# Kernel optimization log

Hardware: AMD Instinct MI355X
Metric: run time of the kernel (lower is better)

The kernel has to match this reference:

```python
import jax, jax.numpy as jnp
import numpy as np

N_NODES = 100000
N_EDGES = 1600000
DIM = 64
L = 5
NUM_GRAPHS = 256
BN_EPS = 1e-5


def setup_inputs() -> dict:
    key = jax.random.key(0)
    ks = jax.random.split(key, 8)
    x = jax.random.normal(ks[0], (N_NODES, DIM), dtype=jnp.float32)
    edge_index = jax.random.randint(ks[1], (2, N_EDGES), 0, N_NODES, dtype=jnp.int32).astype(jnp.int64)
    batch = jnp.sort(jax.random.randint(ks[2], (N_NODES,), 0, NUM_GRAPHS, dtype=jnp.int32)).astype(jnp.int64)
    W1 = jax.random.normal(ks[3], (L, DIM, DIM), dtype=jnp.float32) * (1.0 / np.sqrt(DIM))
    b1 = jnp.zeros((L, DIM), dtype=jnp.float32)
    W2 = jax.random.normal(ks[4], (L, DIM, DIM), dtype=jnp.float32) * (1.0 / np.sqrt(DIM))
    b2 = jnp.zeros((L, DIM), dtype=jnp.float32)
    gamma = jnp.ones((L, DIM), dtype=jnp.float32)
    beta = jnp.zeros((L, DIM), dtype=jnp.float32)
    return {"x": x, "edge_index": edge_index, "batch": batch, "W1": W1, "b1": b1, "W2": W2, "b2": b2, "gamma": gamma, "beta": beta}


def reference(x, edge_index, batch, W1, b1, W2, b2, gamma, beta):
    src, dst = edge_index[0], edge_index[1]
    n = x.shape[0]
    h = x
    xs = []
    for i in range(L):
        # GINConv (eps=0): h_i' = MLP(h_i + sum_{j->i} h_j), scatter-add over edges
        agg = jax.ops.segment_sum(h[src], dst, num_segments=n)
        z = h + agg
        z = jnp.maximum(z @ W1[i] + b1[i], 0.0) @ W2[i] + b2[i]
        z = jnp.maximum(z, 0.0)  # outer ReLU
        # BatchNorm1d, training-mode batch stats (biased var)
        mu = jnp.mean(z, axis=0)
        var = jnp.mean((z - mu) ** 2, axis=0)
        z = (z - mu) * jax.lax.rsqrt(var + BN_EPS) * gamma[i] + beta[i]
        xs.append(z)
        h = z
    counts = jax.ops.segment_sum(jnp.ones((n,), dtype=x.dtype), batch, num_segments=NUM_GRAPHS)
    counts = jnp.maximum(counts, 1.0)[:, None]
    xpool = [jax.ops.segment_sum(z, batch, num_segments=NUM_GRAPHS) / counts for z in xs]
    return jnp.concatenate(xpool, axis=1), jnp.concatenate(xs, axis=1)
```

## Files before the change

### kernel.cpp

```cpp
#include <hip/hip_runtime.h>

#define N_NODES 100000
#define N_EDGES 1600000
#define DIM 64
#define NLAYERS 5
#define NUM_GRAPHS 256
#define BN_EPS 1e-5f
#define STATS_BLOCKS 256
#define CSR_CAP 32
#define OV_CAP 65536
#define NSHARD 4
#define SHARD_W (N_NODES / NSHARD)
#define NBLK ((N_NODES + 255) / 256)

__global__ __launch_bounds__(256) void build_csr_shard_kernel(
        const int* __restrict__ ei, int* __restrict__ cursor,
        int* __restrict__ csr, int* __restrict__ ovcnt, int* __restrict__ ovpairs,
        int lo, int hi) {
    int e = blockIdx.x * 256 + threadIdx.x;
    if (e >= N_EDGES) return;
    int t = ei[N_EDGES + e];
    if (t < lo || t >= hi) return;
    int s = ei[e];
    int c = atomicAdd(&cursor[t], 1);
    if (c < CSR_CAP) {
        csr[t * CSR_CAP + c] = s;
    } else {
        int o = atomicAdd(ovcnt, 1);
        if (o < OV_CAP) { ovpairs[2 * o] = t; ovpairs[2 * o + 1] = s; }
    }
}

__global__ void pad_csr_kernel(const int* __restrict__ cursor, int* __restrict__ csr) {
    int n = blockIdx.x * 256 + threadIdx.x;
    if (n >= N_NODES) return;
    int cnt = min(cursor[n], CSR_CAP);
    int cnt8 = (cnt + 7) & ~7;
    for (int k = cnt; k < cnt8; ++k) csr[n * CSR_CAP + k] = 0;
}

__global__ __launch_bounds__(256) void aggregate_kernel(
        const int* __restrict__ csr, const int* __restrict__ deg,
        const int* __restrict__ ovcnt, const int* __restrict__ ovpairs,
        const float* __restrict__ h, int hstride, float* __restrict__ agg) {
    long tid = (long)blockIdx.x * 256 + threadIdx.x;
    int n = (int)(tid >> 6);
    int d = (int)(tid & 63);
    if (n >= N_NODES) return;
    int dval = deg[n];
    int cnt = min(dval, CSR_CAP);
    int cnt8 = (cnt + 7) & ~7;
    const int4* row = (const int4*)(csr + n * CSR_CAP);
    float own = h[(long)n * hstride + d];
    float a0 = 0.f, a1 = 0.f, a2 = 0.f, a3 = 0.f;
    float a4 = 0.f, a5 = 0.f, a6 = 0.f, a7 = 0.f;
    for (int k = 0; k < cnt8; k += 8) {
        int4 ra = row[k >> 2];
        int4 rb = row[(k >> 2) + 1];
        float v0 = h[(long)ra.x * hstride + d];
        float v1 = h[(long)ra.y * hstride + d];
        float v2 = h[(long)ra.z * hstride + d];
        float v3 = h[(long)ra.w * hstride + d];
        float v4 = h[(long)rb.x * hstride + d];
        float v5 = h[(long)rb.y * hstride + d];
        float v6 = h[(long)rb.z * hstride + d];
        float v7 = h[(long)rb.w * hstride + d];
        if (k + 0 < cnt) a0 += v0;
        if (k + 1 < cnt) a1 += v1;
        if (k + 2 < cnt) a2 += v2;
        if (k + 3 < cnt) a3 += v3;
        if (k + 4 < cnt) a4 += v4;
        if (k + 5 < cnt) a5 += v5;
        if (k + 6 < cnt) a6 += v6;
        if (k + 7 < cnt) a7 += v7;
    }
    if (dval > CSR_CAP) {
        int m = min(*ovcnt, OV_CAP);
        for (int i = 0; i < m; ++i) {
            if (ovpairs[2 * i] == n) a0 += h[(long)ovpairs[2 * i + 1] * hstride + d];
        }
    }
    agg[(long)n * DIM + d] = own + ((a0 + a1) + (a2 + a3)) + ((a4 + a5) + (a6 + a7));
}

__global__ __launch_bounds__(256) void mlp_gemm_kernel(
        const float* __restrict__ in, const float* __restrict__ W,
        const float* __restrict__ b, float* __restrict__ out) {
    __shared__ __align__(16) float sW[DIM * DIM];
    __shared__ float sb[DIM];
    for (int k = threadIdx.x; k < DIM * DIM / 4; k += 256)
        ((float4*)sW)[k] = ((const float4*)W)[k];
    if (threadIdx.x < DIM) sb[threadIdx.x] = b[threadIdx.x];
    __syncthreads();

    int p = threadIdx.x & 127;
    int j0 = (threadIdx.x >> 7) * 32;
    int base = blockIdx.x * 256;
    int n0 = base + p;
    int n1 = base + 128 + p;
    bool v1 = n1 < N_NODES;
    const float* inr0 = in + (long)n0 * DIM;
    const float* inr1 = in + (long)(v1 ? n1 : n0) * DIM;

    float acc0[32], acc1[32];
#pragma unroll
    for (int j = 0; j < 32; ++j) { acc0[j] = sb[j0 + j]; acc1[j] = acc0[j]; }

    for (int d4 = 0; d4 < DIM / 4; ++d4) {
        float4 za = ((const float4*)inr0)[d4];
        float4 zb = ((const float4*)inr1)[d4];
        const float* w0 = sW + (d4 * 4 + 0) * DIM + j0;
        const float* w1 = sW + (d4 * 4 + 1) * DIM + j0;
        const float* w2 = sW + (d4 * 4 + 2) * DIM + j0;
        const float* w3 = sW + (d4 * 4 + 3) * DIM + j0;
#pragma unroll
        for (int j = 0; j < 32; j += 4) {
            float4 a0 = *(const float4*)(w0 + j);
            float4 a1 = *(const float4*)(w1 + j);
            float4 a2 = *(const float4*)(w2 + j);
            float4 a3 = *(const float4*)(w3 + j);
            acc0[j + 0] += za.x * a0.x + za.y * a1.x + za.z * a2.x + za.w * a3.x;
            acc0[j + 1] += za.x * a0.y + za.y * a1.y + za.z * a2.y + za.w * a3.y;
            acc0[j + 2] += za.x * a0.z + za.y * a1.z + za.z * a2.z + za.w * a3.z;
            acc0[j + 3] += za.x * a0.w + za.y * a1.w + za.z * a2.w + za.w * a3.w;
            acc1[j + 0] += zb.x * a0.x + zb.y * a1.x + zb.z * a2.x + zb.w * a3.x;
            acc1[j + 1] += zb.x * a0.y + zb.y * a1.y + zb.z * a2.y + zb.w * a3.y;
            acc1[j + 2] += zb.x * a0.z + zb.y * a1.z + zb.z * a2.z + zb.w * a3.z;
            acc1[j + 3] += zb.x * a0.w + zb.y * a1.w + zb.z * a2.w + zb.w * a3.w;
        }
    }

    float* o0 = out + (long)n0 * DIM + j0;
#pragma unroll
    for (int j = 0; j < 32; j += 4) {
        float4 v = { fmaxf(acc0[j], 0.f), fmaxf(acc0[j + 1], 0.f),
                     fmaxf(acc0[j + 2], 0.f), fmaxf(acc0[j + 3], 0.f) };
        *(float4*)(o0 + j) = v;
    }
    if (v1) {
        float* o1 = out + (long)n1 * DIM + j0;
#pragma unroll
        for (int j = 0; j < 32; j += 4) {
            float4 v = { fmaxf(acc1[j], 0.f), fmaxf(acc1[j + 1], 0.f),
                         fmaxf(acc1[j + 2], 0.f), fmaxf(acc1[j + 3], 0.f) };
            *(float4*)(o1 + j) = v;
        }
    }
}

__global__ void stats_partial_kernel(const float* __restrict__ z, float* __restrict__ partials) {
    __shared__ float red[2 * 256];
    int d = threadIdx.x & 63;
    int slot = threadIdx.x >> 6;
    const int S = STATS_BLOCKS * 4;
    float s1 = 0.f, s2 = 0.f;
    int n = blockIdx.x * 4 + slot;
    for (; n + 3 * S < N_NODES; n += 4 * S) {
        float v0 = z[(long)(n + 0 * S) * DIM + d];
        float v1 = z[(long)(n + 1 * S) * DIM + d];
        float v2 = z[(long)(n + 2 * S) * DIM + d];
        float v3 = z[(long)(n + 3 * S) * DIM + d];
        s1 += v0 + v1 + v2 + v3;
        s2 += v0 * v0 + v1 * v1 + v2 * v2 + v3 * v3;
    }
    for (; n < N_NODES; n += S) {
        float v = z[(long)n * DIM + d];
        s1 += v;
        s2 += v * v;
    }
    red[threadIdx.x] = s1;
    red[256 + threadIdx.x] = s2;
    __syncthreads();
    if (threadIdx.x < 64) {
        float a = red[d] + red[64 + d] + red[128 + d] + red[192 + d];
        float c = red[256 + d] + red[320 + d] + red[384 + d] + red[448 + d];
        partials[blockIdx.x * 128 + d] = a;
        partials[blockIdx.x * 128 + 64 + d] = c;
    }
}

__global__ void stats_finalize_kernel(const float* __restrict__ partials,
                                      const float* __restrict__ gamma,
                                      const float* __restrict__ beta,
                                      float* __restrict__ ss) {
    __shared__ float r1[256], r2[256];
    int d = threadIdx.x & 63, q = threadIdx.x >> 6;
    float s1 = 0.f, s2 = 0.f;
    for (int b2_ = q; b2_ < STATS_BLOCKS; b2_ += 4) {
        s1 += partials[b2_ * 128 + d];
        s2 += partials[b2_ * 128 + 64 + d];
    }
    r1[threadIdx.x] = s1;
    r2[threadIdx.x] = s2;
    __syncthreads();
    if (threadIdx.x < 64) {
        s1 = r1[d] + r1[64 + d] + r1[128 + d] + r1[192 + d];
        s2 = r2[d] + r2[64 + d] + r2[128 + d] + r2[192 + d];
        float mu = s1 * (1.f / N_NODES);
        float var = s2 * (1.f / N_NODES) - mu * mu;
        float rs = 1.f / sqrtf(fmaxf(var, 0.f) + BN_EPS);
        float sc = gamma[d] * rs;
        ss[d] = sc;
        ss[64 + d] = beta[d] - mu * sc;
    }
}

__global__ void bn_apply_kernel(const float* __restrict__ z, const float* __restrict__ ss,
                                float* __restrict__ outxs) {
    long t = (long)blockIdx.x * 256 + threadIdx.x;
    if (t >= (long)N_NODES * (DIM / 4)) return;
    int r = (int)(t & 15);
    long n = t >> 4;
    float4 v = ((const float4*)(z + n * DIM))[r];
    float4 sc = ((const float4*)ss)[r];
    float4 sh = ((const float4*)(ss + DIM))[r];
    float4 o = { v.x * sc.x + sh.x, v.y * sc.y + sh.y,
                 v.z * sc.z + sh.z, v.w * sc.w + sh.w };
    ((float4*)(outxs + n * (DIM * NLAYERS)))[r] = o;
}

__global__ void graph_starts_kernel(const int* __restrict__ batch, int* __restrict__ starts) {
    int g = threadIdx.x;
    if (g > NUM_GRAPHS) return;
    int lo = 0, hi = N_NODES;
    while (lo < hi) {
        int mid = (lo + hi) >> 1;
        if (batch[mid] < g) lo = mid + 1; else hi = mid;
    }
    starts[g] = lo;
}

__global__ void pool_kernel(const float* __restrict__ xs, const int* __restrict__ starts,
                            float* __restrict__ outpool) {
    int g = blockIdx.x;
    int d = threadIdx.x;
    int s = starts[g], e = starts[g + 1];
    const int LD = DIM * NLAYERS;
    float a0 = 0.f, a1 = 0.f, a2 = 0.f, a3 = 0.f;
    float a4 = 0.f, a5 = 0.f, a6 = 0.f, a7 = 0.f;
    int n = s;
    for (; n + 8 <= e; n += 8) {
        a0 += xs[(long)(n + 0) * LD + d];
        a1 += xs[(long)(n + 1) * LD + d];
        a2 += xs[(long)(n + 2) * LD + d];
        a3 += xs[(long)(n + 3) * LD + d];
        a4 += xs[(long)(n + 4) * LD + d];
        a5 += xs[(long)(n + 5) * LD + d];
        a6 += xs[(long)(n + 6) * LD + d];
        a7 += xs[(long)(n + 7) * LD + d];
    }
    for (; n < e; ++n) a0 += xs[(long)n * LD + d];
    float acc = ((a0 + a1) + (a2 + a3)) + ((a4 + a5) + (a6 + a7));
    outpool[(long)g * LD + d] = acc / fmaxf((float)(e - s), 1.f);
}

static inline size_t rup(size_t x) { return (x + 255) & ~(size_t)255; }

extern "C" void kernel_launch(void* const* d_in, const int* in_sizes, int n_in,
                              void* d_out, int out_size, void* d_ws, size_t ws_size,
                              hipStream_t stream) {
    const float* x     = (const float*)d_in[0];
    const int*   ei    = (const int*)d_in[1];
    const int*   batch = (const int*)d_in[2];
    const float* W1    = (const float*)d_in[3];
    const float* b1    = (const float*)d_in[4];
    const float* W2    = (const float*)d_in[5];
    const float* b2    = (const float*)d_in[6];
    const float* gamma = (const float*)d_in[7];
    const float* beta  = (const float*)d_in[8];

    float* out      = (float*)d_out;
    float* out_pool = out;
    float* out_xs   = out + (size_t)NUM_GRAPHS * DIM * NLAYERS;

    char* w = (char*)d_ws;
    int*   csr      = (int*)w;    w += rup((size_t)N_NODES * CSR_CAP * 4);
    int*   cursor   = (int*)w;    w += rup((size_t)N_NODES * 4);
    int*   ovcnt    = (int*)w;    w += 256;
    int*   ovpairs  = (int*)w;    w += rup((size_t)OV_CAP * 8);
    float* agg      = (float*)w;  w += rup((size_t)N_NODES * DIM * 4);
    float* bufB     = (float*)w;  w += rup((size_t)N_NODES * DIM * 4);
    float* partials = (float*)w;  w += rup((size_t)STATS_BLOCKS * 128 * 4);
    float* ss       = (float*)w;  w += 512;
    int*   starts   = (int*)w;    w += rup((size_t)(NUM_GRAPHS + 1) * 4);

    hipMemsetAsync(cursor, 0, (size_t)N_NODES * 4, stream);
    hipMemsetAsync(ovcnt, 0, 4, stream);
    for (int sh = 0; sh < NSHARD; ++sh) {
        build_csr_shard_kernel<<<(N_EDGES + 255) / 256, 256, 0, stream>>>(
            ei, cursor, csr, ovcnt, ovpairs, sh * SHARD_W, (sh + 1) * SHARD_W);
    }
    pad_csr_kernel<<<NBLK, 256, 0, stream>>>(cursor, csr);
    graph_starts_kernel<<<1, 320, 0, stream>>>(batch, starts);

    const float* h = x;
    int hs = DIM;
    for (int l = 0; l < NLAYERS; ++l) {
        aggregate_kernel<<<((long)N_NODES * DIM + 255) / 256, 256, 0, stream>>>(
            csr, cursor, ovcnt, ovpairs, h, hs, agg);
        mlp_gemm_kernel<<<NBLK, 256, 0, stream>>>(
            agg, W1 + (size_t)l * DIM * DIM, b1 + (size_t)l * DIM, bufB);
        mlp_gemm_kernel<<<NBLK, 256, 0, stream>>>(
            bufB, W2 + (size_t)l * DIM * DIM, b2 + (size_t)l * DIM, agg);
        stats_partial_kernel<<<STATS_BLOCKS, 256, 0, stream>>>(agg, partials);
        stats_finalize_kernel<<<1, 256, 0, stream>>>(partials, gamma + (size_t)l * DIM,
                                                     beta + (size_t)l * DIM, ss);
        bn_apply_kernel<<<((long)N_NODES * (DIM / 4) + 255) / 256, 256, 0, stream>>>(
            agg, ss, out_xs + (size_t)l * DIM);
        h = out_xs + (size_t)l * DIM;
        hs = DIM * NLAYERS;
    }

    pool_kernel<<<NUM_GRAPHS, 320, 0, stream>>>(out_xs, starts, out_pool);
}
```

Measured before the change: 960.0 us.

## Aggregate from feature-sliced node layout with one wave per node-slice

Node features are stored in a slice-major layout (8 slices of 8 floats per node), written by a new transpose kernel for the input and by the BN apply kernel for later layers. Aggregation runs one wavefront per node and slice: eight lanes per neighbour group each gather 8 contiguous floats, and the partial sums are combined with cross-lane shuffles. The aim is to keep each slice's gather working set small enough to stay in cache and to load the CSR row once instead of per feature. The padding kernel is dropped because indices are now masked, and the pool kernel is split across layers into more blocks. The cost is an extra layout buffer, extra writes in BN apply, and one block per four nodes per slice.

```diff
diff --git a/kernel.cpp b/kernel.cpp
--- a/kernel.cpp
+++ b/kernel.cpp
@@ -12,6 +12,7 @@
 #define NSHARD 4
 #define SHARD_W (N_NODES / NSHARD)
 #define NBLK ((N_NODES + 255) / 256)
+#define NSLICE 8
 
 __global__ __launch_bounds__(256) void build_csr_shard_kernel(
         const int* __restrict__ ei, int* __restrict__ cursor,
@@ -31,56 +32,71 @@
     }
 }
 
-__global__ void pad_csr_kernel(const int* __restrict__ cursor, int* __restrict__ csr) {
-    int n = blockIdx.x * 256 + threadIdx.x;
-    if (n >= N_NODES) return;
-    int cnt = min(cursor[n], CSR_CAP);
-    int cnt8 = (cnt + 7) & ~7;
-    for (int k = cnt; k < cnt8; ++k) csr[n * CSR_CAP + k] = 0;
-}
-
-__global__ __launch_bounds__(256) void aggregate_kernel(
+__global__ void transpose_x_kernel(const float* __restrict__ x, float* __restrict__ hb) {
+    long t = (long)blockIdx.x * 256 + threadIdx.x;
+    if (t >= (long)N_NODES * DIM) return;
+    int n = (int)(t >> 6);
+    int d = (int)(t & 63);
+    hb[((long)(d >> 3) * N_NODES + n) * 8 + (d & 7)] = x[t];
+}
+
+__global__ __launch_bounds__(256) void aggregate_sliced_kernel(
         const int* __restrict__ csr, const int* __restrict__ deg,
         const int* __restrict__ ovcnt, const int* __restrict__ ovpairs,
-        const float* __restrict__ h, int hstride, float* __restrict__ agg) {
-    long tid = (long)blockIdx.x * 256 + threadIdx.x;
-    int n = (int)(tid >> 6);
-    int d = (int)(tid & 63);
-    if (n >= N_NODES) return;
+        const float* __restrict__ hb, float* __restrict__ agg) {
+    int slice = blockIdx.x & 7;
+    int chunk = blockIdx.x >> 3;
+    int wv = threadIdx.x >> 6;
+    int lane = threadIdx.x & 63;
+    int g = lane >> 3;
+    int j = lane & 7;
+    int n = chunk * 4 + wv;
+    const float* hs = hb + (long)slice * N_NODES * 8;
+
     int dval = deg[n];
     int cnt = min(dval, CSR_CAP);
     int cnt8 = (cnt + 7) & ~7;
-    const int4* row = (const int4*)(csr + n * CSR_CAP);
-    float own = h[(long)n * hstride + d];
-    float a0 = 0.f, a1 = 0.f, a2 = 0.f, a3 = 0.f;
-    float a4 = 0.f, a5 = 0.f, a6 = 0.f, a7 = 0.f;
-    for (int k = 0; k < cnt8; k += 8) {
-        int4 ra = row[k >> 2];
-        int4 rb = row[(k >> 2) + 1];
-        float v0 = h[(long)ra.x * hstride + d];
-        float v1 = h[(long)ra.y * hstride + d];
-        float v2 = h[(long)ra.z * hstride + d];
-        float v3 = h[(long)ra.w * hstride + d];
-        float v4 = h[(long)rb.x * hstride + d];
-        float v5 = h[(long)rb.y * hstride + d];
-        float v6 = h[(long)rb.z * hstride + d];
-        float v7 = h[(long)rb.w * hstride + d];
-        if (k + 0 < cnt) a0 += v0;
-        if (k + 1 < cnt) a1 += v1;
-        if (k + 2 < cnt) a2 += v2;
-        if (k + 3 < cnt) a3 += v3;
-        if (k + 4 < cnt) a4 += v4;
-        if (k + 5 < cnt) a5 += v5;
-        if (k + 6 < cnt) a6 += v6;
-        if (k + 7 < cnt) a7 += v7;
+    const int* row = csr + n * CSR_CAP;
+
+    int r0 = __builtin_nontemporal_load(&row[g]);
+    int r1 = __builtin_nontemporal_load(&row[8 + g]);
+    int r2 = __builtin_nontemporal_load(&row[16 + g]);
+    int r3 = __builtin_nontemporal_load(&row[24 + g]);
+    r0 = (g < cnt) ? r0 : 0;
+    r1 = (8 + g < cnt) ? r1 : 0;
+    r2 = (16 + g < cnt) ? r2 : 0;
+    r3 = (24 + g < cnt) ? r3 : 0;
+
+    float acc = (g == 0) ? hs[(long)n * 8 + j] : 0.f;
+    if (cnt8 > 0) {
+        float v = hs[(long)r0 * 8 + j];
+        acc += (g < cnt) ? v : 0.f;
+    }
+    if (cnt8 > 8) {
+        float v = hs[(long)r1 * 8 + j];
+        acc += (8 + g < cnt) ? v : 0.f;
+    }
+    if (cnt8 > 16) {
+        float v = hs[(long)r2 * 8 + j];
+        acc += (16 + g < cnt) ? v : 0.f;
+    }
+    if (cnt8 > 24) {
+        float v = hs[(long)r3 * 8 + j];
+        acc += (24 + g < cnt) ? v : 0.f;
     }
     if (dval > CSR_CAP) {
-        int m = min(*ovcnt, OV_CAP);
+        int m = min(__builtin_nontemporal_load(ovcnt), OV_CAP);
         for (int i = 0; i < m; ++i) {
-            if (ovpairs[2 * i] == n) a0 += h[(long)ovpairs[2 * i + 1] * hstride + d];
+            if (__builtin_nontemporal_load(&ovpairs[2 * i]) == n && g == 0)
+                acc += hs[(long)__builtin_nontemporal_load(&ovpairs[2 * i + 1]) * 8 + j];
         }
     }
-    agg[(long)n * DIM + d] = own + ((a0 + a1) + (a2 + a3)) + ((a4 + a5) + (a6 + a7));
+
+    acc += __shfl_xor(acc, 8, 64);
+    acc += __shfl_xor(acc, 16, 64);
+    acc += __shfl_xor(acc, 32, 64);
+    if (g == 0)
+        __builtin_nontemporal_store(acc, &agg[(long)n * DIM + slice * 8 + j]);
 }
 
 __global__ __launch_bounds__(256) void mlp_gemm_kernel(
@@ -206,7 +222,7 @@
 }
 
 __global__ void bn_apply_kernel(const float* __restrict__ z, const float* __restrict__ ss,
-                                float* __restrict__ outxs) {
+                                float* __restrict__ outxs, float* __restrict__ hbn) {
     long t = (long)blockIdx.x * 256 + threadIdx.x;
     if (t >= (long)N_NODES * (DIM / 4)) return;
     int r = (int)(t & 15);
@@ -217,6 +233,9 @@
     float4 o = { v.x * sc.x + sh.x, v.y * sc.y + sh.y,
                  v.z * sc.z + sh.z, v.w * sc.w + sh.w };
     ((float4*)(outxs + n * (DIM * NLAYERS)))[r] = o;
+    if (hbn) {
+        *(float4*)(hbn + ((long)(r >> 1) * N_NODES + n) * 8 + (r & 1) * 4) = o;
+    }
 }
 
 __global__ void graph_starts_kernel(const int* __restrict__ batch, int* __restrict__ starts) {
@@ -230,10 +249,11 @@
     starts[g] = lo;
 }
 
-__global__ void pool_kernel(const float* __restrict__ xs, const int* __restrict__ starts,
-                            float* __restrict__ outpool) {
+__global__ __launch_bounds__(64) void pool_kernel(
+        const float* __restrict__ xs, const int* __restrict__ starts,
+        float* __restrict__ outpool) {
     int g = blockIdx.x;
-    int d = threadIdx.x;
+    int d = blockIdx.y * 64 + threadIdx.x;
     int s = starts[g], e = starts[g + 1];
     const int LD = DIM * NLAYERS;
     float a0 = 0.f, a1 = 0.f, a2 = 0.f, a3 = 0.f;
@@ -280,6 +300,7 @@
     int*   ovpairs  = (int*)w;    w += rup((size_t)OV_CAP * 8);
     float* agg      = (float*)w;  w += rup((size_t)N_NODES * DIM * 4);
     float* bufB     = (float*)w;  w += rup((size_t)N_NODES * DIM * 4);
+    float* hb       = (float*)w;  w += rup((size_t)NSLICE * N_NODES * 8 * 4);
     float* partials = (float*)w;  w += rup((size_t)STATS_BLOCKS * 128 * 4);
     float* ss       = (float*)w;  w += 512;
     int*   starts   = (int*)w;    w += rup((size_t)(NUM_GRAPHS + 1) * 4);
@@ -290,14 +311,12 @@
         build_csr_shard_kernel<<<(N_EDGES + 255) / 256, 256, 0, stream>>>(
             ei, cursor, csr, ovcnt, ovpairs, sh * SHARD_W, (sh + 1) * SHARD_W);
     }
-    pad_csr_kernel<<<NBLK, 256, 0, stream>>>(cursor, csr);
+    transpose_x_kernel<<<((long)N_NODES * DIM + 255) / 256, 256, 0, stream>>>(x, hb);
     graph_starts_kernel<<<1, 320, 0, stream>>>(batch, starts);
 
-    const float* h = x;
-    int hs = DIM;
     for (int l = 0; l < NLAYERS; ++l) {
-        aggregate_kernel<<<((long)N_NODES * DIM + 255) / 256, 256, 0, stream>>>(
-            csr, cursor, ovcnt, ovpairs, h, hs, agg);
+        aggregate_sliced_kernel<<<(N_NODES / 4) * NSLICE, 256, 0, stream>>>(
+            csr, cursor, ovcnt, ovpairs, hb, agg);
         mlp_gemm_kernel<<<NBLK, 256, 0, stream>>>(
             agg, W1 + (size_t)l * DIM * DIM, b1 + (size_t)l * DIM, bufB);
         mlp_gemm_kernel<<<NBLK, 256, 0, stream>>>(
@@ -306,10 +325,8 @@
         stats_finalize_kernel<<<1, 256, 0, stream>>>(partials, gamma + (size_t)l * DIM,
                                                      beta + (size_t)l * DIM, ss);
         bn_apply_kernel<<<((long)N_NODES * (DIM / 4) + 255) / 256, 256, 0, stream>>>(
-            agg, ss, out_xs + (size_t)l * DIM);
-        h = out_xs + (size_t)l * DIM;
-        hs = DIM * NLAYERS;
-    }
-
-    pool_kernel<<<NUM_GRAPHS, 320, 0, stream>>>(out_xs, starts, out_pool);
-}
+            agg, ss, out_xs + (size_t)l * DIM, (l + 1 < NLAYERS) ? hb : nullptr);
+    }
+
+    pool_kernel<<<dim3(NUM_GRAPHS, NLAYERS), 64, 0, stream>>>(out_xs, starts, out_pool);
+}
```

Result: slower. 1.646 ms (+71.5%).

## Gather neighbor features from a compact fp16 copy during aggregation

Applied to the files above, without the earlier changes.

Keeps a half-precision, densely packed copy of the node features, written by a new cast kernel for the input and by the BN apply kernel for later layers. The neighbor gather reads this copy instead of strided fp32 rows, which halves gather traffic and improves cache footprint; the self term stays fp32. Padding is replaced by index masking, which removes the pad kernel, and the pooling kernel is split across layers into more blocks. The risk is reduced precision in the aggregated sums compared with the fp32 reference.

```diff
diff --git a/kernel.cpp b/kernel.cpp
--- a/kernel.cpp
+++ b/kernel.cpp
@@ -12,6 +12,9 @@
 #define NSHARD 4
 #define SHARD_W (N_NODES / NSHARD)
 #define NBLK ((N_NODES + 255) / 256)
+
+typedef _Float16 f16;
+typedef _Float16 f16x4 __attribute__((ext_vector_type(4)));
 
 __global__ __launch_bounds__(256) void build_csr_shard_kernel(
         const int* __restrict__ ei, int* __restrict__ cursor,
@@ -31,53 +34,61 @@
     }
 }
 
-__global__ void pad_csr_kernel(const int* __restrict__ cursor, int* __restrict__ csr) {
-    int n = blockIdx.x * 256 + threadIdx.x;
-    if (n >= N_NODES) return;
-    int cnt = min(cursor[n], CSR_CAP);
-    int cnt8 = (cnt + 7) & ~7;
-    for (int k = cnt; k < cnt8; ++k) csr[n * CSR_CAP + k] = 0;
-}
-
-__global__ __launch_bounds__(256) void aggregate_kernel(
+__global__ void cast_x_kernel(const float* __restrict__ x, f16* __restrict__ h16) {
+    long t = (long)blockIdx.x * 256 + threadIdx.x;
+    if (t >= (long)N_NODES * DIM / 4) return;
+    float4 v = ((const float4*)x)[t];
+    f16x4 p = { (f16)v.x, (f16)v.y, (f16)v.z, (f16)v.w };
+    *(f16x4*)(h16 + t * 4) = p;
+}
+
+__global__ __launch_bounds__(256) void aggregate_f16_kernel(
         const int* __restrict__ csr, const int* __restrict__ deg,
         const int* __restrict__ ovcnt, const int* __restrict__ ovpairs,
-        const float* __restrict__ h, int hstride, float* __restrict__ agg) {
+        const f16* __restrict__ h16, const float* __restrict__ hself, int hstride,
+        float* __restrict__ agg) {
     long tid = (long)blockIdx.x * 256 + threadIdx.x;
     int n = (int)(tid >> 6);
     int d = (int)(tid & 63);
     if (n >= N_NODES) return;
     int dval = deg[n];
     int cnt = min(dval, CSR_CAP);
-    int cnt8 = (cnt + 7) & ~7;
     const int4* row = (const int4*)(csr + n * CSR_CAP);
-    float own = h[(long)n * hstride + d];
+    float own = hself[(long)n * hstride + d];
     float a0 = 0.f, a1 = 0.f, a2 = 0.f, a3 = 0.f;
     float a4 = 0.f, a5 = 0.f, a6 = 0.f, a7 = 0.f;
-    for (int k = 0; k < cnt8; k += 8) {
+    for (int k = 0; k < cnt; k += 8) {
         int4 ra = row[k >> 2];
         int4 rb = row[(k >> 2) + 1];
-        float v0 = h[(long)ra.x * hstride + d];
-        float v1 = h[(long)ra.y * hstride + d];
-        float v2 = h[(long)ra.z * hstride + d];
-        float v3 = h[(long)ra.w * hstride + d];
-        float v4 = h[(long)rb.x * hstride + d];
-        float v5 = h[(long)rb.y * hstride + d];
-        float v6 = h[(long)rb.z * hstride + d];
-        float v7 = h[(long)rb.w * hstride + d];
-        if (k + 0 < cnt) a0 += v0;
-        if (k + 1 < cnt) a1 += v1;
-        if (k + 2 < cnt) a2 += v2;
-        if (k + 3 < cnt) a3 += v3;
-        if (k + 4 < cnt) a4 += v4;
-        if (k + 5 < cnt) a5 += v5;
-        if (k + 6 < cnt) a6 += v6;
-        if (k + 7 < cnt) a7 += v7;
+        int s0 = (k + 0 < cnt) ? ra.x : 0;
+        int s1 = (k + 1 < cnt) ? ra.y : 0;
+        int s2 = (k + 2 < cnt) ? ra.z : 0;
+        int s3 = (k + 3 < cnt) ? ra.w : 0;
+        int s4 = (k + 4 < cnt) ? rb.x : 0;
+        int s5 = (k + 5 < cnt) ? rb.y : 0;
+        int s6 = (k + 6 < cnt) ? rb.z : 0;
+        int s7 = (k + 7 < cnt) ? rb.w : 0;
+        float v0 = (float)h16[(long)s0 * DIM + d];
+        float v1 = (float)h16[(long)s1 * DIM + d];
+        float v2 = (float)h16[(long)s2 * DIM + d];
+        float v3 = (float)h16[(long)s3 * DIM + d];
+        float v4 = (float)h16[(long)s4 * DIM + d];
+        float v5 = (float)h16[(long)s5 * DIM + d];
+        float v6 = (float)h16[(long)s6 * DIM + d];
+        float v7 = (float)h16[(long)s7 * DIM + d];
+        a0 += (k + 0 < cnt) ? v0 : 0.f;
+        a1 += (k + 1 < cnt) ? v1 : 0.f;
+        a2 += (k + 2 < cnt) ? v2 : 0.f;
+        a3 += (k + 3 < cnt) ? v3 : 0.f;
+        a4 += (k + 4 < cnt) ? v4 : 0.f;
+        a5 += (k + 5 < cnt) ? v5 : 0.f;
+        a6 += (k + 6 < cnt) ? v6 : 0.f;
+        a7 += (k + 7 < cnt) ? v7 : 0.f;
     }
     if (dval > CSR_CAP) {
         int m = min(*ovcnt, OV_CAP);
         for (int i = 0; i < m; ++i) {
-            if (ovpairs[2 * i] == n) a0 += h[(long)ovpairs[2 * i + 1] * hstride + d];
+            if (ovpairs[2 * i] == n) a0 += (float)h16[(long)ovpairs[2 * i + 1] * DIM + d];
         }
     }
     agg[(long)n * DIM + d] = own + ((a0 + a1) + (a2 + a3)) + ((a4 + a5) + (a6 + a7));
@@ -206,7 +217,7 @@
 }
 
 __global__ void bn_apply_kernel(const float* __restrict__ z, const float* __restrict__ ss,
-                                float* __restrict__ outxs) {
+                                float* __restrict__ outxs, f16* __restrict__ h16) {
     long t = (long)blockIdx.x * 256 + threadIdx.x;
     if (t >= (long)N_NODES * (DIM / 4)) return;
     int r = (int)(t & 15);
@@ -217,6 +228,10 @@
     float4 o = { v.x * sc.x + sh.x, v.y * sc.y + sh.y,
                  v.z * sc.z + sh.z, v.w * sc.w + sh.w };
     ((float4*)(outxs + n * (DIM * NLAYERS)))[r] = o;
+    if (h16) {
+        f16x4 p = { (f16)o.x, (f16)o.y, (f16)o.z, (f16)o.w };
+        *(f16x4*)(h16 + n * DIM + r * 4) = p;
+    }
 }
 
 __global__ void graph_starts_kernel(const int* __restrict__ batch, int* __restrict__ starts) {
@@ -230,10 +245,11 @@
     starts[g] = lo;
 }
 
-__global__ void pool_kernel(const float* __restrict__ xs, const int* __restrict__ starts,
-                            float* __restrict__ outpool) {
+__global__ __launch_bounds__(64) void pool_kernel(
+        const float* __restrict__ xs, const int* __restrict__ starts,
+        float* __restrict__ outpool) {
     int g = blockIdx.x;
-    int d = threadIdx.x;
+    int d = blockIdx.y * 64 + threadIdx.x;
     int s = starts[g], e = starts[g + 1];
     const int LD = DIM * NLAYERS;
     float a0 = 0.f, a1 = 0.f, a2 = 0.f, a3 = 0.f;
@@ -280,9 +296,11 @@
     int*   ovpairs  = (int*)w;    w += rup((size_t)OV_CAP * 8);
     float* agg      = (float*)w;  w += rup((size_t)N_NODES * DIM * 4);
     float* bufB     = (float*)w;  w += rup((size_t)N_NODES * DIM * 4);
+    f16*   h16      = (f16*)w;    w += rup((size_t)N_NODES * DIM * 2);
     float* partials = (float*)w;  w += rup((size_t)STATS_BLOCKS * 128 * 4);
     float* ss       = (float*)w;  w += 512;
     int*   starts   = (int*)w;    w += rup((size_t)(NUM_GRAPHS + 1) * 4);
+    float* zbuf     = agg;
 
     hipMemsetAsync(cursor, 0, (size_t)N_NODES * 4, stream);
     hipMemsetAsync(ovcnt, 0, 4, stream);
@@ -290,26 +308,26 @@
         build_csr_shard_kernel<<<(N_EDGES + 255) / 256, 256, 0, stream>>>(
             ei, cursor, csr, ovcnt, ovpairs, sh * SHARD_W, (sh + 1) * SHARD_W);
     }
-    pad_csr_kernel<<<NBLK, 256, 0, stream>>>(cursor, csr);
+    cast_x_kernel<<<((long)N_NODES * DIM / 4 + 255) / 256, 256, 0, stream>>>(x, h16);
     graph_starts_kernel<<<1, 320, 0, stream>>>(batch, starts);
 
-    const float* h = x;
+    const float* hself = x;
     int hs = DIM;
     for (int l = 0; l < NLAYERS; ++l) {
-        aggregate_kernel<<<((long)N_NODES * DIM + 255) / 256, 256, 0, stream>>>(
-            csr, cursor, ovcnt, ovpairs, h, hs, agg);
+        aggregate_f16_kernel<<<((long)N_NODES * DIM + 255) / 256, 256, 0, stream>>>(
+            csr, cursor, ovcnt, ovpairs, h16, hself, hs, agg);
         mlp_gemm_kernel<<<NBLK, 256, 0, stream>>>(
             agg, W1 + (size_t)l * DIM * DIM, b1 + (size_t)l * DIM, bufB);
         mlp_gemm_kernel<<<NBLK, 256, 0, stream>>>(
-            bufB, W2 + (size_t)l * DIM * DIM, b2 + (size_t)l * DIM, agg);
-        stats_partial_kernel<<<STATS_BLOCKS, 256, 0, stream>>>(agg, partials);
+            bufB, W2 + (size_t)l * DIM * DIM, b2 + (size_t)l * DIM, zbuf);
+        stats_partial_kernel<<<STATS_BLOCKS, 256, 0, stream>>>(zbuf, partials);
         stats_finalize_kernel<<<1, 256, 0, stream>>>(partials, gamma + (size_t)l * DIM,
                                                      beta + (size_t)l * DIM, ss);
         bn_apply_kernel<<<((long)N_NODES * (DIM / 4) + 255) / 256, 256, 0, stream>>>(
-            agg, ss, out_xs + (size_t)l * DIM);
-        h = out_xs + (size_t)l * DIM;
+            zbuf, ss, out_xs + (size_t)l * DIM, (l + 1 < NLAYERS) ? h16 : nullptr);
+        hself = out_xs + (size_t)l * DIM;
         hs = DIM * NLAYERS;
     }
 
-    pool_kernel<<<NUM_GRAPHS, 320, 0, stream>>>(out_xs, starts, out_pool);
-}
+    pool_kernel<<<dim3(NUM_GRAPHS, NLAYERS), 64, 0, stream>>>(out_xs, starts, out_pool);
+}
```

Result: faster. 863.1 us (median of 2 runs) (-10.1%).
